# Performance work log

Hardware: AMD Instinct MI355X
Metric: run time of the kernel (lower is better)

The kernel has to match this reference:

```python
import jax, jax.numpy as jnp
import numpy as np

B, T, M, P = 256, 128, 64, 64


def setup_inputs() -> dict:
    key = jax.random.key(0)
    ks = jax.random.split(key, 20)
    s = 0.05
    inp = {
        "data": jax.random.normal(ks[0], (B, T - 1, 1), jnp.float32),
        "encoder_h": jax.random.normal(ks[1], (B, T, M), jnp.float32),
        "h0": jax.random.normal(ks[2], (B, P), jnp.float32),
        "s0": jax.random.normal(ks[3], (B, P), jnp.float32),
        # dense: Dense(1) on concat([x, context]) -> in=1+M
        "W_dense": jax.random.normal(ks[4], (1 + M, 1), jnp.float32) * s,
        "b_dense": jnp.zeros((1,), jnp.float32),
        # LSTM(p): kernel (1,4p), recurrent (p,4p), bias (4p); keras gate order i,f,c,o
        "Wk": jax.random.normal(ks[5], (1, 4 * P), jnp.float32) * s,
        "Uk": jax.random.normal(ks[6], (P, 4 * P), jnp.float32) * s,
        "bk": jnp.zeros((4 * P,), jnp.float32),
        # temporal attention: W_d Dense(m) on concat([h,c]) (2p -> m)
        "Wd": jax.random.normal(ks[7], (2 * P, M), jnp.float32) * s,
        "bWd": jnp.zeros((M,), jnp.float32),
        # U_d Dense(m) on encoder_h (m -> m)
        "Ud": jax.random.normal(ks[8], (M, M), jnp.float32) * s,
        "bUd": jnp.zeros((M,), jnp.float32),
        # v_d Dense(1)
        "vd": jax.random.normal(ks[9], (M, 1), jnp.float32) * s,
        "bvd": jnp.zeros((1,), jnp.float32),
        # dense_vb: Dense(1) on concat([h, context]) (p+m -> 1)
        "Wvb": jax.random.normal(ks[10], (P + M, 1), jnp.float32) * s,
        "bvb": jnp.zeros((1,), jnp.float32),
        # dense_Wb: Dense(p) applied AFTER dense_vb (1 -> p), as in the source
        "Wb": jax.random.normal(ks[11], (1, P), jnp.float32) * s,
        "bWb": jnp.zeros((P,), jnp.float32),
    }
    return inp


def reference(data, encoder_h, h0, s0, W_dense, b_dense, Wk, Uk, bk,
              Wd, bWd, Ud, bUd, vd, bvd, Wvb, bvb, Wb, bWb):
    # Loop-invariant: U_d(encoder_h), (B,T,M). Math identical to per-step compute.
    Ue = jnp.einsum('btm,mn->btn', encoder_h, Ud) + bUd

    def step(carry, x_t):
        ctx, _h = carry                      # ctx: (B,M)
        inp = jnp.concatenate([x_t, ctx], axis=-1)   # (B, 1+M)
        y = inp @ W_dense + b_dense                   # (B,1)
        # NOTE: source resets LSTM state to (h0, s0) at every step.
        z = y @ Wk + h0 @ Uk + bk                     # (B,4P)
        i_g, f_g, g_g, o_g = jnp.split(z, 4, axis=-1)
        c = jax.nn.sigmoid(f_g) * s0 + jax.nn.sigmoid(i_g) * jnp.tanh(g_g)
        h = jax.nn.sigmoid(o_g) * jnp.tanh(c)         # (B,P)
        # temporal attention
        dproj = jnp.concatenate([h, c], axis=-1) @ Wd + bWd   # (B,M)
        e = jnp.tanh(dproj[:, None, :] + Ue) @ vd + bvd        # (B,T,1)
        beta = jax.nn.softmax(e, axis=1)                       # (B,T,1)
        ctx_new = jnp.einsum('bti,btm->bm', beta, encoder_h)   # (B,M)
        return (ctx_new, h), None

    Bsz = encoder_h.shape[0]
    carry0 = (jnp.zeros((Bsz, Wk.shape[1] // 4 * 0 + encoder_h.shape[2]), encoder_h.dtype),
              jnp.zeros((Bsz, Uk.shape[0]), encoder_h.dtype))
    xs = jnp.transpose(data, (1, 0, 2))  # (T-1, B, 1)
    (ctx, h), _ = jax.lax.scan(step, carry0, xs)

    concatenated = jnp.concatenate([h, ctx], axis=-1)[:, None, :]  # (B,1,P+M)
    out = (concatenated @ Wvb + bvb) @ Wb + bWb                     # (B,1,P)
    return out
```

## Files before the change

kernel.cpp:

```cpp
#include <hip/hip_runtime.h>


#define Bn 256
#define Tn 128
#define Mn 64
#define Pn 64
#define NTH 256
#define NW 4
#define UST 68
#define DPST 72
#define K2C 2.885390081777927f

typedef float f32x2 __attribute__((ext_vector_type(2)));

__device__ __forceinline__ float fexp(float x) {
    return __builtin_amdgcn_exp2f(x * 1.44269504088896341f);
}
__device__ __forceinline__ float fexp2(float x) { return __builtin_amdgcn_exp2f(x); }
__device__ __forceinline__ float frcp(float x) { return __builtin_amdgcn_rcpf(x); }
__device__ __forceinline__ float fsig(float x) { return frcp(1.0f + fexp(-x)); }
__device__ __forceinline__ float ftanh(float x) { return 1.0f - 2.0f * frcp(1.0f + fexp(2.0f * x)); }

template <int CTRL>
__device__ __forceinline__ float dppmov(float x) {
    return __int_as_float(__builtin_amdgcn_update_dpp(
        0, __float_as_int(x), CTRL, 0xf, 0xf, false));
}
__device__ __forceinline__ float rdlane(float x, int l) {
    return __int_as_float(__builtin_amdgcn_readlane(__float_as_int(x), l));
}
__device__ __forceinline__ float wavesum63(float x) {
    x += dppmov<0x111>(x);
    x += dppmov<0x112>(x);
    x += dppmov<0x114>(x);
    x += dppmov<0x118>(x);
    x += dppmov<0x142>(x);
    x += dppmov<0x143>(x);
    return x;
}

#define OFF_ENC   0
#define OFF_UD    8704
#define OFF_PRE   13056
#define OFF_DPW   13312
#define OFF_YSDEN 13600
#define OFF_CTXP  13616
#define SMEM_FLOATS 13872

__global__ __launch_bounds__(NTH, 1)
void decoder_kernel(const float* __restrict__ data, const float* __restrict__ enc,
                    const float* __restrict__ h0, const float* __restrict__ s0,
                    const float* __restrict__ W_dense, const float* __restrict__ b_dense,
                    const float* __restrict__ Wk, const float* __restrict__ Uk,
                    const float* __restrict__ bk,
                    const float* __restrict__ Wd, const float* __restrict__ bWd,
                    const float* __restrict__ Ud, const float* __restrict__ bUd,
                    const float* __restrict__ vd, const float* __restrict__ bvd,
                    const float* __restrict__ Wvb, const float* __restrict__ bvb,
                    const float* __restrict__ Wb, const float* __restrict__ bWb,
                    float* __restrict__ out)
{
    extern __shared__ float smem[];
    float* enc_s  = smem + OFF_ENC;
    float* Ud_s   = smem + OFF_UD;
    float* pre_s  = smem + OFF_PRE;
    float* dprojw = smem + OFF_DPW;
    f32x2* ysden  = (f32x2*)(smem + OFF_YSDEN);
    float* ctxp   = smem + OFF_CTXP;

    const int b    = blockIdx.x;
    const int tid  = threadIdx.x;
    const int lane = tid & 63;
    const int wv   = tid >> 6;

    {
        const float* encg = enc + (size_t)b * Tn * Mn;
        #pragma unroll
        for (int i = 0; i < 8; i++) {
            int flat = (i * NTH + tid) * 4;
            int t = flat >> 6, m = flat & 63;
            *(float4*)(enc_s + t * UST + m) = *(const float4*)(encg + flat);
        }
        #pragma unroll
        for (int i = 0; i < 4; i++) {
            int flat = (i * NTH + tid) * 4;
            int k = flat >> 6, n = flat & 63;
            *(float4*)(Ud_s + k * UST + n) = *(const float4*)(Ud + flat);
        }
        {
            float s = bk[tid];
            const float* h0b = h0 + b * Pn;
            #pragma unroll
            for (int k = 0; k < Pn; k++) s = fmaf(h0b[k], Uk[k * 4 * Pn + tid], s);
            pre_s[tid] = s;
        }
        if (tid < 2 * NW) {
            f32x2 z; z.x = 0.0f; z.y = 0.25f;
            ysden[tid] = z;
        }
    }
    __syncthreads();

    const int t_e = tid >> 1, q_e = tid & 1, m0 = q_e * 32;
    f32x2 ue2[16];
    {
        float acc[32];
        #pragma unroll
        for (int j = 0; j < 32; j++) acc[j] = bUd[m0 + j];
        for (int k = 0; k < Mn; k++) {
            float a = enc_s[t_e * UST + k];
            const float4* ud = (const float4*)(Ud_s + k * UST + m0);
            #pragma unroll
            for (int j4 = 0; j4 < 8; j4++) {
                float4 u = ud[j4];
                acc[4 * j4 + 0] = fmaf(a, u.x, acc[4 * j4 + 0]);
                acc[4 * j4 + 1] = fmaf(a, u.y, acc[4 * j4 + 1]);
                acc[4 * j4 + 2] = fmaf(a, u.z, acc[4 * j4 + 2]);
                acc[4 * j4 + 3] = fmaf(a, u.w, acc[4 * j4 + 3]);
            }
        }
        #pragma unroll
        for (int j = 0; j < 16; j++) {
            ue2[j].x = K2C * acc[2 * j];
            ue2[j].y = K2C * acc[2 * j + 1];
        }
    }

    float enc_r[32];
    #pragma unroll
    for (int j = 0; j < 32; j++)
        enc_r[j] = enc_s[(32 * wv + j) * UST + lane];
    float wd_r[128];
    #pragma unroll
    for (int k = 0; k < 128; k++)
        wd_r[k] = K2C * Wd[k * Mn + lane];
    const float W0  = W_dense[0];
    const float bd  = b_dense[0];
    const float Wde = W_dense[1 + lane];
    const float wk_i = Wk[lane], wk_f = Wk[64 + lane],
                wk_g = Wk[128 + lane], wk_o = Wk[192 + lane];
    const float s0v   = s0[b * Pn + lane];
    const float bvd0  = bvd[0];
    const float bwd_l = K2C * bWd[lane];
    f32x2 vd2[16];
    float sumvd32 = 0.0f;
    #pragma unroll
    for (int j = 0; j < 16; j++) {
        float va = vd[m0 + 2 * j], vb = vd[m0 + 2 * j + 1];
        vd2[j].x = -2.0f * va; vd2[j].y = -2.0f * vb;
        sumvd32 += va + vb;
    }
    const float pre_i = pre_s[lane];
    const float pre_f = pre_s[64 + lane];
    const float pre_g = pre_s[128 + lane];
    const float pre_o = pre_s[192 + lane];
    const float* xb = data + (size_t)b * (Tn - 1);
    const float x_lo = xb[lane];
    const float x_hi = (lane < 63) ? xb[64 + lane] : 0.0f;

    float h = 0.0f, c = 0.0f;
    float* dp_my = dprojw + wv * DPST;

    for (int st = 0; st < Tn - 1; ++st) {
        const int par = st & 1, nxt = par ^ 1;

        f32x2 yv = ysden[par * NW + (lane & 3)];
        yv.x += dppmov<0x111>(yv.x); yv.y += dppmov<0x111>(yv.y);
        yv.x += dppmov<0x112>(yv.x); yv.y += dppmov<0x112>(yv.y);
        float ytot = rdlane(yv.x, 3);
        float dtot = rdlane(yv.y, 3);
        float xs = (st < 64) ? rdlane(x_lo, st) : rdlane(x_hi, st - 64);
        float y = fmaf(xs, W0, fmaf(ytot, frcp(dtot), bd));

        float zi = fmaf(y, wk_i, pre_i);
        float zf = fmaf(y, wk_f, pre_f);
        float zg = fmaf(y, wk_g, pre_g);
        float zo = fmaf(y, wk_o, pre_o);
        c = fsig(zf) * s0v + fsig(zi) * ftanh(zg);
        h = fsig(zo) * ftanh(c);

        {
            float p0 = 0.0f, p1 = 0.0f, p2 = 0.0f, p3 = 0.0f;
            #pragma unroll
            for (int k = 0; k < 16; k++) {
                p0 = fmaf(rdlane(h, 4 * k + 0), wd_r[4 * k + 0], p0);
                p1 = fmaf(rdlane(h, 4 * k + 1), wd_r[4 * k + 1], p1);
                p2 = fmaf(rdlane(h, 4 * k + 2), wd_r[4 * k + 2], p2);
                p3 = fmaf(rdlane(h, 4 * k + 3), wd_r[4 * k + 3], p3);
            }
            #pragma unroll
            for (int k = 0; k < 16; k++) {
                p0 = fmaf(rdlane(c, 4 * k + 0), wd_r[64 + 4 * k + 0], p0);
                p1 = fmaf(rdlane(c, 4 * k + 1), wd_r[64 + 4 * k + 1], p1);
                p2 = fmaf(rdlane(c, 4 * k + 2), wd_r[64 + 4 * k + 2], p2);
                p3 = fmaf(rdlane(c, 4 * k + 3), wd_r[64 + 4 * k + 3], p3);
            }
            dp_my[lane] = ((p0 + p1) + (p2 + p3)) + bwd_l;
        }

        float ex;
        {
            float4 d[8];
            const float4* dp4 = (const float4*)(dp_my + m0);
            #pragma unroll
            for (int i = 0; i < 8; i++) d[i] = dp4[i];
            f32x2 accA; accA.x = sumvd32; accA.y = 0.0f;
            f32x2 accB; accB.x = 0.0f;    accB.y = 0.0f;
            #pragma unroll
            for (int i = 0; i < 8; i++) {
                f32x2 sA, rA, sB, rB;
                sA.x = d[i].x + ue2[2 * i].x;     sA.y = d[i].y + ue2[2 * i].y;
                rA.x = frcp(1.0f + fexp2(sA.x));  rA.y = frcp(1.0f + fexp2(sA.y));
                accA += vd2[2 * i] * rA;
                sB.x = d[i].z + ue2[2 * i + 1].x; sB.y = d[i].w + ue2[2 * i + 1].y;
                rB.x = frcp(1.0f + fexp2(sB.x));  rB.y = frcp(1.0f + fexp2(sB.y));
                accB += vd2[2 * i + 1] * rB;
            }
            f32x2 accT = accA + accB;
            float acc = accT.x + accT.y;
            acc += dppmov<0x111>(acc);
            ex = fexp(acc + bvd0);
        }

        {
            float p0 = 0.0f, p1 = 0.0f, p2 = 0.0f, p3 = 0.0f;
            #pragma unroll
            for (int j = 0; j < 8; j++) {
                p0 = fmaf(rdlane(ex, 2 * j + 1),        enc_r[j],      p0);
                p1 = fmaf(rdlane(ex, 2 * (j + 8) + 1),  enc_r[8 + j],  p1);
                p2 = fmaf(rdlane(ex, 2 * (j + 16) + 1), enc_r[16 + j], p2);
                p3 = fmaf(rdlane(ex, 2 * (j + 24) + 1), enc_r[24 + j], p3);
            }
            float ctxpart = (p0 + p1) + (p2 + p3);
            if (st == Tn - 2) ctxp[wv * 64 + lane] = ctxpart;
            f32x2 w2;
            w2.x = ctxpart * Wde;
            w2.y = (lane & 1) ? ex : 0.0f;
            w2.x += dppmov<0x111>(w2.x); w2.y += dppmov<0x111>(w2.y);
            w2.x += dppmov<0x112>(w2.x); w2.y += dppmov<0x112>(w2.y);
            w2.x += dppmov<0x114>(w2.x); w2.y += dppmov<0x114>(w2.y);
            w2.x += dppmov<0x118>(w2.x); w2.y += dppmov<0x118>(w2.y);
            w2.x += dppmov<0x142>(w2.x); w2.y += dppmov<0x142>(w2.y);
            w2.x += dppmov<0x143>(w2.x); w2.y += dppmov<0x143>(w2.y);
            if (lane == 63) ysden[nxt * NW + wv] = w2;
        }
        __syncthreads();
    }

    if (wv == 0) {
        float dtot = ysden[NW + 0].y + ysden[NW + 1].y
                   + ysden[NW + 2].y + ysden[NW + 3].y;
        float invS = frcp(dtot);
        float ctxm = 0.0f;
        #pragma unroll
        for (int w = 0; w < NW; w++) ctxm += ctxp[w * 64 + lane];
        ctxm *= invS;
        float part = h * Wvb[lane] + ctxm * Wvb[64 + lane];
        float v = rdlane(wavesum63(part), 63) + bvb[0];
        out[(size_t)b * Pn + lane] = fmaf(v, Wb[lane], bWb[lane]);
    }
}

extern "C" void kernel_launch(void* const* d_in, const int* in_sizes, int n_in,
                              void* d_out, int out_size, void* d_ws, size_t ws_size,
                              hipStream_t stream) {
    const float* data    = (const float*)d_in[0];
    const float* enc     = (const float*)d_in[1];
    const float* h0      = (const float*)d_in[2];
    const float* s0      = (const float*)d_in[3];
    const float* W_dense = (const float*)d_in[4];
    const float* b_dense = (const float*)d_in[5];
    const float* Wk      = (const float*)d_in[6];
    const float* Uk      = (const float*)d_in[7];
    const float* bk      = (const float*)d_in[8];
    const float* Wd      = (const float*)d_in[9];
    const float* bWd     = (const float*)d_in[10];
    const float* Ud      = (const float*)d_in[11];
    const float* bUd     = (const float*)d_in[12];
    const float* vd      = (const float*)d_in[13];
    const float* bvd     = (const float*)d_in[14];
    const float* Wvb     = (const float*)d_in[15];
    const float* bvb     = (const float*)d_in[16];
    const float* Wb      = (const float*)d_in[17];
    const float* bWb     = (const float*)d_in[18];

    decoder_kernel<<<Bn, NTH, SMEM_FLOATS * sizeof(float), stream>>>(
        data, enc, h0, s0, W_dense, b_dense, Wk, Uk, bk,
        Wd, bWd, Ud, bUd, vd, bvd, Wvb, bvb, Wb, bWb, (float*)d_out);
}
```

Measured before the change: 283.7 us.

## Double waves per block and use LDS broadcast for attention projection

Raises the block from 4 to 8 waves so each wave covers 16 timesteps of the attention instead of 32, halving per-wave exp/rcp work and the context reduction per step. The h/c vector is now written to per-wave LDS and read back as float4 broadcasts instead of 128 readlane operations for the W_d projection. In exchange, every one of the 127 steps synchronises twice as many waves, the LSTM gates and W_d projection are computed redundantly in each wave, and register pressure must fit launch bounds of 512 threads.

```diff
diff --git a/kernel.cpp b/kernel.cpp
--- a/kernel.cpp
+++ b/kernel.cpp
@@ -5,10 +5,11 @@
 #define Tn 128
 #define Mn 64
 #define Pn 64
-#define NTH 256
-#define NW 4
+#define NTH 512
+#define NW 8
 #define UST 68
 #define DPST 72
+#define HCST 132
 #define K2C 2.885390081777927f
 
 typedef float f32x2 __attribute__((ext_vector_type(2)));
@@ -43,11 +44,12 @@
 #define OFF_UD    8704
 #define OFF_PRE   13056
 #define OFF_DPW   13312
-#define OFF_YSDEN 13600
-#define OFF_CTXP  13616
-#define SMEM_FLOATS 13872
-
-__global__ __launch_bounds__(NTH, 1)
+#define OFF_HC    13888
+#define OFF_YSDEN 14944
+#define OFF_CTXP  14976
+#define SMEM_FLOATS 15488
+
+__global__ __launch_bounds__(NTH, 2)
 void decoder_kernel(const float* __restrict__ data, const float* __restrict__ enc,
                     const float* __restrict__ h0, const float* __restrict__ s0,
                     const float* __restrict__ W_dense, const float* __restrict__ b_dense,
@@ -65,6 +67,7 @@
     float* Ud_s   = smem + OFF_UD;
     float* pre_s  = smem + OFF_PRE;
     float* dprojw = smem + OFF_DPW;
+    float* hcw    = smem + OFF_HC;
     f32x2* ysden  = (f32x2*)(smem + OFF_YSDEN);
     float* ctxp   = smem + OFF_CTXP;
 
@@ -76,18 +79,18 @@
     {
         const float* encg = enc + (size_t)b * Tn * Mn;
         #pragma unroll
-        for (int i = 0; i < 8; i++) {
+        for (int i = 0; i < 4; i++) {
             int flat = (i * NTH + tid) * 4;
             int t = flat >> 6, m = flat & 63;
             *(float4*)(enc_s + t * UST + m) = *(const float4*)(encg + flat);
         }
         #pragma unroll
-        for (int i = 0; i < 4; i++) {
+        for (int i = 0; i < 2; i++) {
             int flat = (i * NTH + tid) * 4;
             int k = flat >> 6, n = flat & 63;
             *(float4*)(Ud_s + k * UST + n) = *(const float4*)(Ud + flat);
         }
-        {
+        if (tid < 4 * Pn) {
             float s = bk[tid];
             const float* h0b = h0 + b * Pn;
             #pragma unroll
@@ -95,23 +98,23 @@
             pre_s[tid] = s;
         }
         if (tid < 2 * NW) {
-            f32x2 z; z.x = 0.0f; z.y = 0.25f;
+            f32x2 z; z.x = 0.0f; z.y = 0.125f;
             ysden[tid] = z;
         }
     }
     __syncthreads();
 
-    const int t_e = tid >> 1, q_e = tid & 1, m0 = q_e * 32;
-    f32x2 ue2[16];
+    const int t_e = 16 * wv + (lane >> 2), q_e = lane & 3, m0 = q_e * 16;
+    f32x2 ue2[8];
     {
-        float acc[32];
-        #pragma unroll
-        for (int j = 0; j < 32; j++) acc[j] = bUd[m0 + j];
+        float acc[16];
+        #pragma unroll
+        for (int j = 0; j < 16; j++) acc[j] = bUd[m0 + j];
         for (int k = 0; k < Mn; k++) {
             float a = enc_s[t_e * UST + k];
             const float4* ud = (const float4*)(Ud_s + k * UST + m0);
             #pragma unroll
-            for (int j4 = 0; j4 < 8; j4++) {
+            for (int j4 = 0; j4 < 4; j4++) {
                 float4 u = ud[j4];
                 acc[4 * j4 + 0] = fmaf(a, u.x, acc[4 * j4 + 0]);
                 acc[4 * j4 + 1] = fmaf(a, u.y, acc[4 * j4 + 1]);
@@ -120,16 +123,16 @@
             }
         }
         #pragma unroll
-        for (int j = 0; j < 16; j++) {
+        for (int j = 0; j < 8; j++) {
             ue2[j].x = K2C * acc[2 * j];
             ue2[j].y = K2C * acc[2 * j + 1];
         }
     }
 
-    float enc_r[32];
+    float enc_r[16];
     #pragma unroll
-    for (int j = 0; j < 32; j++)
-        enc_r[j] = enc_s[(32 * wv + j) * UST + lane];
+    for (int j = 0; j < 16; j++)
+        enc_r[j] = enc_s[(16 * wv + j) * UST + lane];
     float wd_r[128];
     #pragma unroll
     for (int k = 0; k < 128; k++)
@@ -142,13 +145,13 @@
     const float s0v   = s0[b * Pn + lane];
     const float bvd0  = bvd[0];
     const float bwd_l = K2C * bWd[lane];
-    f32x2 vd2[16];
-    float sumvd32 = 0.0f;
+    f32x2 vd2[8];
+    float sumvd16 = 0.0f;
     #pragma unroll
-    for (int j = 0; j < 16; j++) {
+    for (int j = 0; j < 8; j++) {
         float va = vd[m0 + 2 * j], vb = vd[m0 + 2 * j + 1];
         vd2[j].x = -2.0f * va; vd2[j].y = -2.0f * vb;
-        sumvd32 += va + vb;
+        sumvd16 += va + vb;
     }
     const float pre_i = pre_s[lane];
     const float pre_f = pre_s[64 + lane];
@@ -160,15 +163,17 @@
 
     float h = 0.0f, c = 0.0f;
     float* dp_my = dprojw + wv * DPST;
+    float* hc_my = hcw + wv * HCST;
 
     for (int st = 0; st < Tn - 1; ++st) {
         const int par = st & 1, nxt = par ^ 1;
 
-        f32x2 yv = ysden[par * NW + (lane & 3)];
+        f32x2 yv = ysden[par * NW + (lane & 7)];
         yv.x += dppmov<0x111>(yv.x); yv.y += dppmov<0x111>(yv.y);
         yv.x += dppmov<0x112>(yv.x); yv.y += dppmov<0x112>(yv.y);
-        float ytot = rdlane(yv.x, 3);
-        float dtot = rdlane(yv.y, 3);
+        yv.x += dppmov<0x114>(yv.x); yv.y += dppmov<0x114>(yv.y);
+        float ytot = rdlane(yv.x, 7);
+        float dtot = rdlane(yv.y, 7);
         float xs = (st < 64) ? rdlane(x_lo, st) : rdlane(x_hi, st - 64);
         float y = fmaf(xs, W0, fmaf(ytot, frcp(dtot), bd));
 
@@ -180,34 +185,30 @@
         h = fsig(zo) * ftanh(c);
 
         {
+            hc_my[lane] = h;
+            hc_my[64 + lane] = c;
             float p0 = 0.0f, p1 = 0.0f, p2 = 0.0f, p3 = 0.0f;
             #pragma unroll
-            for (int k = 0; k < 16; k++) {
-                p0 = fmaf(rdlane(h, 4 * k + 0), wd_r[4 * k + 0], p0);
-                p1 = fmaf(rdlane(h, 4 * k + 1), wd_r[4 * k + 1], p1);
-                p2 = fmaf(rdlane(h, 4 * k + 2), wd_r[4 * k + 2], p2);
-                p3 = fmaf(rdlane(h, 4 * k + 3), wd_r[4 * k + 3], p3);
-            }
-            #pragma unroll
-            for (int k = 0; k < 16; k++) {
-                p0 = fmaf(rdlane(c, 4 * k + 0), wd_r[64 + 4 * k + 0], p0);
-                p1 = fmaf(rdlane(c, 4 * k + 1), wd_r[64 + 4 * k + 1], p1);
-                p2 = fmaf(rdlane(c, 4 * k + 2), wd_r[64 + 4 * k + 2], p2);
-                p3 = fmaf(rdlane(c, 4 * k + 3), wd_r[64 + 4 * k + 3], p3);
+            for (int k4 = 0; k4 < 32; k4++) {
+                float4 hv = *(const float4*)(hc_my + 4 * k4);
+                p0 = fmaf(hv.x, wd_r[4 * k4 + 0], p0);
+                p1 = fmaf(hv.y, wd_r[4 * k4 + 1], p1);
+                p2 = fmaf(hv.z, wd_r[4 * k4 + 2], p2);
+                p3 = fmaf(hv.w, wd_r[4 * k4 + 3], p3);
             }
             dp_my[lane] = ((p0 + p1) + (p2 + p3)) + bwd_l;
         }
 
         float ex;
         {
-            float4 d[8];
+            float4 d[4];
             const float4* dp4 = (const float4*)(dp_my + m0);
             #pragma unroll
-            for (int i = 0; i < 8; i++) d[i] = dp4[i];
-            f32x2 accA; accA.x = sumvd32; accA.y = 0.0f;
+            for (int i = 0; i < 4; i++) d[i] = dp4[i];
+            f32x2 accA; accA.x = sumvd16; accA.y = 0.0f;
             f32x2 accB; accB.x = 0.0f;    accB.y = 0.0f;
             #pragma unroll
-            for (int i = 0; i < 8; i++) {
+            for (int i = 0; i < 4; i++) {
                 f32x2 sA, rA, sB, rB;
                 sA.x = d[i].x + ue2[2 * i].x;     sA.y = d[i].y + ue2[2 * i].y;
                 rA.x = frcp(1.0f + fexp2(sA.x));  rA.y = frcp(1.0f + fexp2(sA.y));
@@ -219,23 +220,24 @@
             f32x2 accT = accA + accB;
             float acc = accT.x + accT.y;
             acc += dppmov<0x111>(acc);
+            acc += dppmov<0x112>(acc);
             ex = fexp(acc + bvd0);
         }
 
         {
             float p0 = 0.0f, p1 = 0.0f, p2 = 0.0f, p3 = 0.0f;
             #pragma unroll
-            for (int j = 0; j < 8; j++) {
-                p0 = fmaf(rdlane(ex, 2 * j + 1),        enc_r[j],      p0);
-                p1 = fmaf(rdlane(ex, 2 * (j + 8) + 1),  enc_r[8 + j],  p1);
-                p2 = fmaf(rdlane(ex, 2 * (j + 16) + 1), enc_r[16 + j], p2);
-                p3 = fmaf(rdlane(ex, 2 * (j + 24) + 1), enc_r[24 + j], p3);
+            for (int j = 0; j < 4; j++) {
+                p0 = fmaf(rdlane(ex, 4 * j + 3),        enc_r[j],      p0);
+                p1 = fmaf(rdlane(ex, 4 * (j + 4) + 3),  enc_r[4 + j],  p1);
+                p2 = fmaf(rdlane(ex, 4 * (j + 8) + 3),  enc_r[8 + j],  p2);
+                p3 = fmaf(rdlane(ex, 4 * (j + 12) + 3), enc_r[12 + j], p3);
             }
             float ctxpart = (p0 + p1) + (p2 + p3);
             if (st == Tn - 2) ctxp[wv * 64 + lane] = ctxpart;
             f32x2 w2;
             w2.x = ctxpart * Wde;
-            w2.y = (lane & 1) ? ex : 0.0f;
+            w2.y = ((lane & 3) == 3) ? ex : 0.0f;
             w2.x += dppmov<0x111>(w2.x); w2.y += dppmov<0x111>(w2.y);
             w2.x += dppmov<0x112>(w2.x); w2.y += dppmov<0x112>(w2.y);
             w2.x += dppmov<0x114>(w2.x); w2.y += dppmov<0x114>(w2.y);
@@ -248,8 +250,9 @@
     }
 
     if (wv == 0) {
-        float dtot = ysden[NW + 0].y + ysden[NW + 1].y
-                   + ysden[NW + 2].y + ysden[NW + 3].y;
+        float dtot = 0.0f;
+        #pragma unroll
+        for (int w = 0; w < NW; w++) dtot += ysden[NW + w].y;
         float invS = frcp(dtot);
         float ctxm = 0.0f;
         #pragma unroll
```

Measured after the change: 295.1 us. 1.04x slower.
